# Performance work log

Measured on AMD Instinct MI355X. Metric: run time of the kernel, lower is better.

The kernel has to match this reference:

```python
import jax, jax.numpy as jnp
import numpy as np

NEG = -1e9  # finite stand-in for -inf mask fill (scores are bounded by |v|_1)


def sparsemax(z):
    """Sparsemax over last axis (Martins & Astudillo 2016)."""
    zs = jnp.sort(z, axis=-1)[..., ::-1]                      # descending
    cs = jnp.cumsum(zs, axis=-1)
    k = jnp.arange(1, z.shape[-1] + 1, dtype=z.dtype)
    support = 1.0 + k * zs > cs
    ksz = jnp.sum(support, axis=-1, keepdims=True)            # support size >= 1
    cs_k = jnp.take_along_axis(cs, ksz.astype(jnp.int32) - 1, axis=-1)
    tau = (cs_k - 1.0) / ksz.astype(z.dtype)
    return jnp.maximum(z - tau, 0.0)


def bahdanau_head(query, values, mask, Wk, Wq, v):
    # query: [B,1,H], values: [B,S,K], mask: [B,1,S]
    proj_keys = values @ Wk                                   # [B,S,H] (precomputed keys)
    proj_q = query @ Wq                                       # [B,1,H]
    scores = jnp.einsum('bsh,h->bs', jnp.tanh(proj_q + proj_keys), v)[:, None, :]  # [B,1,S]
    scores = jnp.where(mask, scores, NEG)
    alphas = sparsemax(scores)                                # [B,1,S]
    context = alphas @ values                                 # [B,1,K]
    return context, alphas


def setup_inputs() -> dict:
    B, S, K, H = 32, 4096, 512, 512
    key = jax.random.key(0)
    ks = jax.random.split(key, 16)
    sc = lambda d: 1.0 / np.sqrt(d)
    mk = lambda k, shp: (jax.random.uniform(k, shp) < 0.95).at[..., 0].set(True)
    return {
        'query': jax.random.normal(ks[0], (B, 1, H), jnp.float32),
        'values_a': jax.random.normal(ks[1], (B, S, K), jnp.float32),
        'values_b': jax.random.normal(ks[2], (B, S, K), jnp.float32),
        'mask_a': mk(ks[3], (B, 1, S)),
        'mask_b': mk(ks[4], (B, 1, S)),
        'Wk_a': jax.random.normal(ks[5], (K, H), jnp.float32) * sc(K),
        'Wq_a': jax.random.normal(ks[6], (H, H), jnp.float32) * sc(H),
        'v_a': jax.random.normal(ks[7], (H,), jnp.float32) * sc(H),
        'Wk_b': jax.random.normal(ks[8], (K, H), jnp.float32) * sc(K),
        'Wq_b': jax.random.normal(ks[9], (H, H), jnp.float32) * sc(H),
        'v_b': jax.random.normal(ks[10], (H,), jnp.float32) * sc(H),
        'Wg': jax.random.normal(ks[11], (H + 2 * K, 2), jnp.float32) * sc(H + 2 * K),
        'bg': jnp.zeros((2,), jnp.float32),
        'Wu_a': jax.random.normal(ks[12], (K + H, H), jnp.float32) * sc(K + H),
        'bu_a': jnp.zeros((H,), jnp.float32),
        'Wu_b': jax.random.normal(ks[13], (K + H, H), jnp.float32) * sc(K + H),
        'bu_b': jnp.zeros((H,), jnp.float32),
    }


def reference(query, values_a, values_b, mask_a, mask_b,
              Wk_a, Wq_a, v_a, Wk_b, Wq_b, v_b,
              Wg, bg, Wu_a, bu_a, Wu_b, bu_b):
    ctx_a, al_a = bahdanau_head(query, values_a, mask_a, Wk_a, Wq_a, v_a)
    ctx_b, al_b = bahdanau_head(query, values_b, mask_b, Wk_b, Wq_b, v_b)
    # AttentionGate merge
    gate_in = jnp.concatenate([query, ctx_a, ctx_b], axis=2)          # [B,1,H+2K]
    gate_w = jax.nn.softmax(gate_in @ Wg + bg, axis=-1)               # [B,1,2]
    cand_a = jnp.tanh(jnp.concatenate([query, ctx_a], axis=2) @ Wu_a + bu_a)  # [B,1,H]
    cand_b = jnp.tanh(jnp.concatenate([query, ctx_b], axis=2) @ Wu_b + bu_b)
    cands = jnp.concatenate([cand_a, cand_b], axis=1)                 # [B,2,H]
    att_vector = gate_w @ cands                                       # [B,1,H]
    return att_vector, al_a, al_b
```

## Files before the change

kernel.cpp:

```cpp
#include <hip/hip_runtime.h>
#include <math.h>

#define NEGV (-1e9f)
constexpr int B = 32, S = 4096, K = 512, H = 512;

typedef __attribute__((ext_vector_type(8))) short bf16x8;
typedef __attribute__((ext_vector_type(4))) float f32x4;
typedef __attribute__((ext_vector_type(4))) int i32x4;

__device__ __forceinline__ short f2bf(float x) {
  union { float f; unsigned u; } v; v.f = x;
  unsigned r = (v.u + 0x7FFFu + ((v.u >> 16) & 1u)) >> 16;
  return (short)r;
}

__device__ __forceinline__ unsigned cvt_pk_bf16(float lo, float hi) {
  unsigned r;
  asm("v_cvt_pk_bf16_f32 %0, %1, %2" : "=v"(r) : "v"(lo), "v"(hi));
  return r;
}

__device__ __forceinline__ void cvt_store16(short* dst, const float4 a, const float4 b) {
  i32x4 t;
  t[0] = (int)cvt_pk_bf16(a.x, a.y);
  t[1] = (int)cvt_pk_bf16(a.z, a.w);
  t[2] = (int)cvt_pk_bf16(b.x, b.y);
  t[3] = (int)cvt_pk_bf16(b.z, b.w);
  *(i32x4*)dst = t;
}

__device__ __forceinline__ float fast_tanh(float x) {
  return 1.f - 2.f / (__expf(2.f * x) + 1.f);
}

__global__ __launch_bounds__(64)
void wkswizzle_kernel(const float* __restrict__ Wk_a, const float* __restrict__ Wk_b,
                      short* __restrict__ WkT) {
  const int head = blockIdx.y;
  const float* __restrict__ Wk = head ? Wk_b : Wk_a;
  const int cn = blockIdx.x;
  const int c = cn >> 5, n = cn & 31;
  const int l = threadIdx.x;
  const int kb = c * 32 + ((l >> 4) << 3);
  const int h = n * 16 + (l & 15);
  bf16x8 frag;
#pragma unroll
  for (int j = 0; j < 8; ++j) frag[j] = f2bf(Wk[(size_t)(kb + j) * H + h]);
  *(bf16x8*)(WkT + (size_t)head * 262144 + ((size_t)cn * 64 + l) * 8) = frag;
}

__global__ __launch_bounds__(512)
void qproj_kernel(const float* __restrict__ query,
                  const float* __restrict__ Wq_a,
                  const float* __restrict__ Wq_b,
                  float* __restrict__ qproj) {
  const int b = blockIdx.x, head = blockIdx.y;
  const float* __restrict__ Wq = head ? Wq_b : Wq_a;
  __shared__ float qs[H];
  qs[threadIdx.x] = query[b * H + threadIdx.x];
  __syncthreads();
  const int h = threadIdx.x;
  float acc = 0.f;
#pragma unroll 8
  for (int k = 0; k < H; ++k) acc = fmaf(qs[k], Wq[k * H + h], acc);
  qproj[(head * B + b) * H + h] = acc;
}

__global__ __launch_bounds__(512, 2)
void scores_mfma_kernel(const float* __restrict__ values_a, const float* __restrict__ values_b,
                        const short* __restrict__ WkT,
                        const float* __restrict__ v_a, const float* __restrict__ v_b,
                        const float* __restrict__ qproj,
                        float* __restrict__ scores) {
  const int head = blockIdx.z, b = blockIdx.y;
  const int s0 = blockIdx.x * 64;
  const float* __restrict__ V  = (head ? values_b : values_a) + (size_t)b * S * K;
  const float* __restrict__ v  = head ? v_b : v_a;
  const float* __restrict__ qp = qproj + (head * B + b) * H;
  const short* __restrict__ wkb = WkT + (size_t)head * 262144;

  __shared__ __align__(16) short Albuf[2][4096];
  __shared__ float red[8 * 64];

  const int tid = threadIdx.x;
  const int w = tid >> 6, l = tid & 63;

  const int sa = tid >> 3, ka = (tid & 7) * 8;
  const float* const arow = V + (size_t)(s0 + sa) * K + ka;
  const int aline = (((ka >> 5) * 4 + (sa >> 4)) * 64 + ((sa & 15) | (((ka & 31) >> 3) << 4))) * 8;
  const short* const bbase = wkb + ((w * 4) * 64 + l) * 8;

  f32x4 acc[4][4] = {};

  float4 pfa[2], pfb[2];
  pfa[0] = *(const float4*)(arow);
  pfb[0] = *(const float4*)(arow + 4);
  pfa[1] = *(const float4*)(arow + 64);
  pfb[1] = *(const float4*)(arow + 68);
  cvt_store16(&Albuf[0][aline], pfa[0], pfb[0]);

#pragma unroll
  for (int c = 0; c < 8; ++c) {
    bf16x8 bfr[2][4];
#pragma unroll
    for (int kk = 0; kk < 2; ++kk)
#pragma unroll
      for (int nl = 0; nl < 4; ++nl)
        bfr[kk][nl] = *(const bf16x8*)(bbase + ((2 * c + kk) * 32 + nl) * 512);
    if (c < 6) {
      pfa[c & 1] = *(const float4*)(arow + (c + 2) * 64);
      pfb[c & 1] = *(const float4*)(arow + (c + 2) * 64 + 4);
    }
    __syncthreads();
#pragma unroll
    for (int kk = 0; kk < 2; ++kk) {
      bf16x8 afr[4];
#pragma unroll
      for (int i = 0; i < 4; ++i)
        afr[i] = *(const bf16x8*)(&Albuf[c & 1][((kk * 4 + i) * 64 + l) * 8]);
#pragma unroll
      for (int nl = 0; nl < 4; ++nl)
#pragma unroll
        for (int i = 0; i < 4; ++i)
          acc[i][nl] = __builtin_amdgcn_mfma_f32_16x16x32_bf16(afr[i], bfr[kk][nl], acc[i][nl], 0, 0, 0);
    }
    if (c < 7) cvt_store16(&Albuf[(c & 1) ^ 1][aline], pfa[(c + 1) & 1], pfb[(c + 1) & 1]);
  }

  float qpr[4], vr[4];
#pragma unroll
  for (int nl = 0; nl < 4; ++nl) {
    const int h = (w * 4 + nl) * 16 + (l & 15);
    qpr[nl] = qp[h];
    vr[nl] = v[h];
  }
#pragma unroll
  for (int i = 0; i < 4; ++i)
#pragma unroll
    for (int r = 0; r < 4; ++r) {
      float p = 0.f;
#pragma unroll
      for (int nl = 0; nl < 4; ++nl) p = fmaf(vr[nl], fast_tanh(acc[i][nl][r] + qpr[nl]), p);
#pragma unroll
      for (int off = 8; off > 0; off >>= 1) p += __shfl_xor(p, off, 64);
      if ((l & 15) == 0) red[w * 64 + i * 16 + (l >> 4) * 4 + r] = p;
    }
  __syncthreads();
  if (tid < 64) {
    float tot = 0.f;
#pragma unroll
    for (int ww = 0; ww < 8; ++ww) tot += red[ww * 64 + tid];
    scores[((size_t)head * B + b) * S + s0 + tid] = tot;
  }
}

__device__ __forceinline__ float bred256(float v, const bool is_max, float* lds) {
#pragma unroll
  for (int o = 32; o > 0; o >>= 1) {
    const float t = __shfl_xor(v, o, 64);
    v = is_max ? fmaxf(v, t) : (v + t);
  }
  __syncthreads();
  if ((threadIdx.x & 63) == 0) lds[threadIdx.x >> 6] = v;
  __syncthreads();
  return is_max ? fmaxf(fmaxf(lds[0], lds[1]), fmaxf(lds[2], lds[3]))
                : (lds[0] + lds[1]) + (lds[2] + lds[3]);
}

__global__ __launch_bounds__(256)
void sparsemax_kernel(const float* __restrict__ scores,
                      const int* __restrict__ mask_a, const int* __restrict__ mask_b,
                      float* __restrict__ d_out_f) {
  const int b = blockIdx.x, head = blockIdx.y;
  const float* __restrict__ z = scores + ((size_t)head * B + b) * S;
  const int* __restrict__ mask = (head ? mask_b : mask_a) + b * S;
  float* __restrict__ alpha = d_out_f + B * H + (size_t)head * B * S + (size_t)b * S;
  __shared__ float lds[4];
  const int tid = threadIdx.x;
  float e[16];
#pragma unroll
  for (int t = 0; t < 16; ++t) {
    const int s = t * 256 + tid;
    e[t] = mask[s] ? z[s] : NEGV;
  }
  float m = NEGV;
#pragma unroll
  for (int t = 0; t < 16; ++t) m = fmaxf(m, e[t]);
  m = bred256(m, true, lds);
  float lo = m - 1.f, hi = m;
  for (int it = 0; it < 28; ++it) {
    const float mid = 0.5f * (lo + hi);
    float s = 0.f;
#pragma unroll
    for (int t = 0; t < 16; ++t) s += fmaxf(e[t] - mid, 0.f);
    s = bred256(s, false, lds);
    if (s >= 1.f) lo = mid; else hi = mid;
  }
  float cnt = 0.f, sum = 0.f;
#pragma unroll
  for (int t = 0; t < 16; ++t) {
    if (e[t] > lo) { cnt += 1.f; sum += e[t]; }
  }
  cnt = bred256(cnt, false, lds);
  sum = bred256(sum, false, lds);
  const float tau = (sum - 1.f) / cnt;
#pragma unroll
  for (int t = 0; t < 16; ++t) alpha[t * 256 + tid] = fmaxf(e[t] - tau, 0.f);
}

__global__ __launch_bounds__(512)
void context_kernel(const float* __restrict__ values_a, const float* __restrict__ values_b,
                    const float* __restrict__ d_out_f, float* __restrict__ ctx) {
  const int b = blockIdx.x, head = blockIdx.y;
  const float* __restrict__ V = (head ? values_b : values_a) + (size_t)b * S * K;
  const float* __restrict__ al = d_out_f + B * H + (size_t)head * B * S + (size_t)b * S;
  __shared__ int cnt;
  __shared__ int sidx[S];
  __shared__ float sal[S];
  if (threadIdx.x == 0) cnt = 0;
  __syncthreads();
  for (int i = threadIdx.x; i < S; i += 512) {
    const float a = al[i];
    if (a > 0.f) { const int p = atomicAdd(&cnt, 1); sidx[p] = i; sal[p] = a; }
  }
  __syncthreads();
  const int n = cnt;
  const int j = threadIdx.x;
  float acc = 0.f;
  for (int t = 0; t < n; ++t) acc = fmaf(sal[t], V[(size_t)sidx[t] * K + j], acc);
  ctx[(head * B + b) * K + j] = acc;
}

__global__ __launch_bounds__(512)
void merge_kernel(const float* __restrict__ query, const float* __restrict__ ctx,
                  const float* __restrict__ Wg, const float* __restrict__ bg,
                  const float* __restrict__ Wu_a, const float* __restrict__ bu_a,
                  const float* __restrict__ Wu_b, const float* __restrict__ bu_b,
                  float* __restrict__ att) {
  const int b = blockIdx.x;
  __shared__ float gin[1536];
  __shared__ float lred[16];
  __shared__ float gw[2];
  const int tid = threadIdx.x;
  gin[tid]        = query[b * H + tid];
  gin[512 + tid]  = ctx[(0 * B + b) * K + tid];
  gin[1024 + tid] = ctx[(1 * B + b) * K + tid];
  __syncthreads();
  float p0 = 0.f, p1 = 0.f;
  for (int i = tid; i < 1536; i += 512) {
    const float x = gin[i];
    p0 = fmaf(x, Wg[i * 2 + 0], p0);
    p1 = fmaf(x, Wg[i * 2 + 1], p1);
  }
#pragma unroll
  for (int o = 32; o > 0; o >>= 1) { p0 += __shfl_xor(p0, o, 64); p1 += __shfl_xor(p1, o, 64); }
  if ((tid & 63) == 0) { lred[tid >> 6] = p0; lred[8 + (tid >> 6)] = p1; }
  __syncthreads();
  if (tid == 0) {
    float l0 = bg[0], l1 = bg[1];
    for (int w = 0; w < 8; ++w) { l0 += lred[w]; l1 += lred[8 + w]; }
    const float mx = fmaxf(l0, l1);
    const float e0 = expf(l0 - mx), e1 = expf(l1 - mx);
    gw[0] = e0 / (e0 + e1);
    gw[1] = e1 / (e0 + e1);
  }
  __syncthreads();
  const int h = tid;
  float aa = bu_a[h], ab = bu_b[h];
  for (int i = 0; i < 1024; ++i) aa = fmaf(gin[i], Wu_a[i * H + h], aa);
  for (int i = 0; i < 1024; ++i) {
    const float x = (i < 512) ? gin[i] : gin[i + 512];
    ab = fmaf(x, Wu_b[i * H + h], ab);
  }
  att[b * H + h] = gw[0] * tanhf(aa) + gw[1] * tanhf(ab);
}

extern "C" void kernel_launch(void* const* d_in, const int* in_sizes, int n_in,
                              void* d_out, int out_size, void* d_ws, size_t ws_size,
                              hipStream_t stream) {
  const float* query    = (const float*)d_in[0];
  const float* values_a = (const float*)d_in[1];
  const float* values_b = (const float*)d_in[2];
  const int*   mask_a   = (const int*)d_in[3];
  const int*   mask_b   = (const int*)d_in[4];
  const float* Wk_a = (const float*)d_in[5];
  const float* Wq_a = (const float*)d_in[6];
  const float* v_a  = (const float*)d_in[7];
  const float* Wk_b = (const float*)d_in[8];
  const float* Wq_b = (const float*)d_in[9];
  const float* v_b  = (const float*)d_in[10];
  const float* Wg   = (const float*)d_in[11];
  const float* bg   = (const float*)d_in[12];
  const float* Wu_a = (const float*)d_in[13];
  const float* bu_a = (const float*)d_in[14];
  const float* Wu_b = (const float*)d_in[15];
  const float* bu_b = (const float*)d_in[16];
  float* out = (float*)d_out;

  float* wsf    = (float*)d_ws;
  float* qproj  = wsf;
  float* scores = wsf + 2 * B * H;
  float* ctx    = wsf + 2 * B * H + 2 * B * S;
  short* WkT    = (short*)(wsf + 2 * B * H + 2 * B * S + 2 * B * K);

  wkswizzle_kernel<<<dim3(512, 2), 64, 0, stream>>>(Wk_a, Wk_b, WkT);
  qproj_kernel<<<dim3(B, 2), 512, 0, stream>>>(query, Wq_a, Wq_b, qproj);
  scores_mfma_kernel<<<dim3(S / 64, B, 2), 512, 0, stream>>>(
      values_a, values_b, WkT, v_a, v_b, qproj, scores);
  sparsemax_kernel<<<dim3(B, 2), 256, 0, stream>>>(scores, mask_a, mask_b, out);
  context_kernel<<<dim3(B, 2), 512, 0, stream>>>(values_a, values_b, out, ctx);
  merge_kernel<<<B, 512, 0, stream>>>(query, ctx, Wg, bg, Wu_a, bu_a, Wu_b, bu_b, out);
}
```

Before: 846.6 us.

## Swizzle LDS A tile, deepen global prefetch, and reorder barriers in score GEMM

Applies an XOR swizzle to the shared-memory layout of the bf16 A tile on both write and read to cut LDS bank conflicts. The global-load prefetch of values rows grows from two stages to three. The barrier moves to after the next-buffer store, using a custom lgkmcnt wait plus s_barrier, and all A fragments are loaded before the MFMA burst, which runs at raised wave priority. The aim is to hide global latency and LDS stalls, at the cost of more registers and some risk of losing occupancy.

```diff
diff --git a/kernel.cpp b/kernel.cpp
--- a/kernel.cpp
+++ b/kernel.cpp
@@ -31,6 +31,12 @@
 
 __device__ __forceinline__ float fast_tanh(float x) {
   return 1.f - 2.f / (__expf(2.f * x) + 1.f);
+}
+
+__device__ __forceinline__ void block_sync_lds() {
+  asm volatile("s_waitcnt lgkmcnt(0)" ::: "memory");
+  __builtin_amdgcn_s_barrier();
+  __builtin_amdgcn_sched_barrier(0);
 }
 
 __global__ __launch_bounds__(64)
@@ -87,17 +93,21 @@
 
   const int sa = tid >> 3, ka = (tid & 7) * 8;
   const float* const arow = V + (size_t)(s0 + sa) * K + ka;
-  const int aline = (((ka >> 5) * 4 + (sa >> 4)) * 64 + ((sa & 15) | (((ka & 31) >> 3) << 4))) * 8;
+  const int g_w = (ka >> 3) & 3, kk_w = ka >> 5;
+  const int Lw = ((kk_w * 4 + (sa >> 4)) * 64 + ((sa & 15) | (g_w << 4))) ^ (g_w | (kk_w << 2));
+  const int aline = Lw * 8;
+  const int rslot0 = l ^ ((l >> 4) & 3);
+  const int rslot1 = rslot0 ^ 4;
   const short* const bbase = wkb + ((w * 4) * 64 + l) * 8;
 
   f32x4 acc[4][4] = {};
 
-  float4 pfa[2], pfb[2];
-  pfa[0] = *(const float4*)(arow);
-  pfb[0] = *(const float4*)(arow + 4);
-  pfa[1] = *(const float4*)(arow + 64);
-  pfb[1] = *(const float4*)(arow + 68);
-  cvt_store16(&Albuf[0][aline], pfa[0], pfb[0]);
+  float4 pa[3], pb[3];
+  pa[0] = *(const float4*)(arow);        pb[0] = *(const float4*)(arow + 4);
+  pa[1] = *(const float4*)(arow + 64);   pb[1] = *(const float4*)(arow + 68);
+  pa[2] = *(const float4*)(arow + 128);  pb[2] = *(const float4*)(arow + 132);
+  cvt_store16(&Albuf[0][aline], pa[0], pb[0]);
+  block_sync_lds();
 
 #pragma unroll
   for (int c = 0; c < 8; ++c) {
@@ -107,24 +117,29 @@
 #pragma unroll
       for (int nl = 0; nl < 4; ++nl)
         bfr[kk][nl] = *(const bf16x8*)(bbase + ((2 * c + kk) * 32 + nl) * 512);
-    if (c < 6) {
-      pfa[c & 1] = *(const float4*)(arow + (c + 2) * 64);
-      pfb[c & 1] = *(const float4*)(arow + (c + 2) * 64 + 4);
+    if (c < 5) {
+      pa[c % 3] = *(const float4*)(arow + (c + 3) * 64);
+      pb[c % 3] = *(const float4*)(arow + (c + 3) * 64 + 4);
     }
-    __syncthreads();
-#pragma unroll
-    for (int kk = 0; kk < 2; ++kk) {
-      bf16x8 afr[4];
-#pragma unroll
-      for (int i = 0; i < 4; ++i)
-        afr[i] = *(const bf16x8*)(&Albuf[c & 1][((kk * 4 + i) * 64 + l) * 8]);
+    bf16x8 afr[2][4];
+#pragma unroll
+    for (int i = 0; i < 4; ++i) {
+      afr[0][i] = *(const bf16x8*)(&Albuf[c & 1][((0 * 4 + i) * 64 + rslot0) * 8]);
+      afr[1][i] = *(const bf16x8*)(&Albuf[c & 1][((1 * 4 + i) * 64 + rslot1) * 8]);
+    }
+    __builtin_amdgcn_s_setprio(1);
+#pragma unroll
+    for (int kk = 0; kk < 2; ++kk)
 #pragma unroll
       for (int nl = 0; nl < 4; ++nl)
 #pragma unroll
         for (int i = 0; i < 4; ++i)
-          acc[i][nl] = __builtin_amdgcn_mfma_f32_16x16x32_bf16(afr[i], bfr[kk][nl], acc[i][nl], 0, 0, 0);
+          acc[i][nl] = __builtin_amdgcn_mfma_f32_16x16x32_bf16(afr[kk][i], bfr[kk][nl], acc[i][nl], 0, 0, 0);
+    __builtin_amdgcn_s_setprio(0);
+    if (c < 7) {
+      cvt_store16(&Albuf[(c & 1) ^ 1][aline], pa[(c + 1) % 3], pb[(c + 1) % 3]);
+      block_sync_lds();
     }
-    if (c < 7) cvt_store16(&Albuf[(c & 1) ^ 1][aline], pfa[(c + 1) & 1], pfb[(c + 1) & 1]);
   }
 
   float qpr[4], vr[4];
```

After: 879.0 us. 1.04x slower.
